# Optimization experiments

Measured on AMD Instinct MI355X. Metric: run time of the kernel, lower is better.

## Reference

```python
import jax, jax.numpy as jnp
from jax import lax
import numpy as np

B, S, D = 4, 4096, 1024
ESCAPE_RADIUS = 2.0  # Mandelbrot-style escape bound used for per-row clamping
EPS = 1e-12


def setup_inputs() -> dict:
    key = jax.random.key(0)
    ks = jax.random.split(key, 6)
    x = jax.random.normal(ks[0], (B, S, D), dtype=jnp.float32)
    gamma = jnp.ones((D,), dtype=jnp.float32)
    beta = jnp.zeros((D,), dtype=jnp.float32)
    scale = 1.0 / np.sqrt(D)
    W_in = jax.random.normal(ks[1], (D, D), dtype=jnp.float32) * scale
    b_in = jnp.zeros((D,), dtype=jnp.float32)
    W_out = jax.random.normal(ks[2], (D, D), dtype=jnp.float32) * scale
    b_out = jnp.zeros((D,), dtype=jnp.float32)
    return {"x": x, "gamma": gamma, "beta": beta, "W_in": W_in,
            "b_in": b_in, "W_out": W_out, "b_out": b_out}


def _layernorm(x, gamma, beta):
    mu = jnp.mean(x, axis=-1, keepdims=True)
    var = jnp.mean((x - mu) ** 2, axis=-1, keepdims=True)
    return (x - mu) * lax.rsqrt(var + 1e-5) * gamma + beta


def _complex_square(z):
    # last dim = [real | imag] halves (torch chunk(2, dim=-1))
    re, im = jnp.split(z, 2, axis=-1)
    return jnp.concatenate([re * re - im * im, 2.0 * re * im], axis=-1)


def reference(x, gamma, beta, W_in, b_in, W_out, b_out):
    h = _layernorm(x, gamma, beta)
    c = jnp.einsum('bsd,de->bse', h, W_in) + b_in  # per-token complex offset

    def step(z, c_t):
        z_raw = _complex_square(z) + c_t
        # per-row L2 norm clamp to escape radius (keeps the chaotic map bounded)
        n = jnp.sqrt(jnp.sum(z_raw * z_raw, axis=-1, keepdims=True) + EPS)
        z_new = z_raw * (ESCAPE_RADIUS / jnp.maximum(n, ESCAPE_RADIUS))
        return z_new, z_new

    c_t_major = jnp.swapaxes(c, 0, 1)  # [S, B, D]
    z0 = jnp.zeros((x.shape[0], x.shape[-1]), dtype=x.dtype)
    _, ys = lax.scan(step, z0, c_t_major)  # ys: [S, B, D]
    y = jnp.swapaxes(ys, 0, 1)  # [B, S, D]
    out = jnp.einsum('bsd,de->bse', y, W_out) + b_out
    return x + out  # residual
```

## Files before the change

### kernel.cpp

```cpp
#include <hip/hip_runtime.h>

typedef __bf16 bf16_t;
typedef float  f32x4  __attribute__((ext_vector_type(4)));
typedef long   longx2 __attribute__((ext_vector_type(2)));
typedef unsigned char u8;
typedef unsigned long long u64;

#define B_DIM 4
#define S_DIM 4096
#define D_DIM 1024
#define M_DIM (B_DIM * S_DIM)

#define CHUNK 32
#define WARM  16

__device__ __forceinline__ int pperm(int k) {
  return (k & ~63) | (((k >> 3) & 3) << 4) | (((k >> 5) & 1) << 3) | (k & 7);
}

__device__ __forceinline__ void g2l16(const void* g, void* l) {
  __builtin_amdgcn_global_load_lds(
      (const __attribute__((address_space(1))) void*)g,
      (__attribute__((address_space(3))) void*)l, 16, 0, 0);
}

__global__ __launch_bounds__(64) void ln_kernel(
    const float* __restrict__ x, const float* __restrict__ gamma,
    const float* __restrict__ beta, u8* __restrict__ h) {
  const int row  = blockIdx.x;
  const int lane = threadIdx.x;
  const float4* xr = (const float4*)(x + (size_t)row * D_DIM);
  float4 v[4];
  float s = 0.f, s2 = 0.f;
#pragma unroll
  for (int j = 0; j < 4; ++j) {
    v[j] = xr[j * 64 + lane];
    s += v[j].x + v[j].y + v[j].z + v[j].w;
    s2 = fmaf(v[j].x, v[j].x, s2);
    s2 = fmaf(v[j].y, v[j].y, s2);
    s2 = fmaf(v[j].z, v[j].z, s2);
    s2 = fmaf(v[j].w, v[j].w, s2);
  }
#pragma unroll
  for (int off = 32; off; off >>= 1) {
    s  += __shfl_xor(s, off);
    s2 += __shfl_xor(s2, off);
  }
  const float mu  = s * (1.f / (float)D_DIM);
  const float var = fmaf(-mu, mu, s2 * (1.f / (float)D_DIM));
  const float inv = rsqrtf(var + 1e-5f);
  int* hr = (int*)(h + (size_t)row * D_DIM);
#pragma unroll
  for (int j = 0; j < 4; ++j) {
    const float4 g4 = ((const float4*)gamma)[j * 64 + lane];
    const float4 b4 = ((const float4*)beta)[j * 64 + lane];
    const float o0 = fmaf((v[j].x - mu) * inv, g4.x, b4.x);
    const float o1 = fmaf((v[j].y - mu) * inv, g4.y, b4.y);
    const float o2 = fmaf((v[j].z - mu) * inv, g4.z, b4.z);
    const float o3 = fmaf((v[j].w - mu) * inv, g4.w, b4.w);
    int p = __builtin_amdgcn_cvt_pk_fp8_f32(o0, o1, 0, false);
    p = __builtin_amdgcn_cvt_pk_fp8_f32(o2, o3, p, true);
    hr[pperm(j * 256 + lane * 4) >> 2] = p;
  }
}

__global__ __launch_bounds__(256) void transpose_fp8_kernel(
    const float* __restrict__ W, u8* __restrict__ WT) {
  __shared__ float tile[32][33];
  const int tx = threadIdx.x & 31;
  const int ty = threadIdx.x >> 5;
  const int bn = blockIdx.x * 32;
  const int bk = blockIdx.y * 32;
#pragma unroll
  for (int i = 0; i < 32; i += 8)
    tile[ty + i][tx] = W[(size_t)(bk + ty + i) * D_DIM + bn + tx];
  __syncthreads();
#pragma unroll
  for (int i = 0; i < 32; i += 8) {
    const int p =
        __builtin_amdgcn_cvt_pk_fp8_f32(16.f * tile[tx][ty + i], 0.f, 0, false);
    WT[(size_t)(bn + ty + i) * D_DIM + pperm(bk + tx)] = (u8)(p & 0xff);
  }
}

#define NTK 16
#define BUFSZ 24576

#define VMCNT(n) asm volatile("s_waitcnt vmcnt(" #n ")" ::: "memory")
#define DSRX(d, a, off) \
  asm volatile("ds_read_b128 %0, %1 offset:" #off : "=v"(d) : "v"(a))

template <int MODE>
__global__ __launch_bounds__(512, 4) void gemm_fp8_kernel(
    const u8* __restrict__ A, const u8* __restrict__ BT,
    const float* __restrict__ bias, const float* __restrict__ xres,
    void* __restrict__ Cout) {
  __shared__ __attribute__((aligned(16))) char lds[3][BUFSZ];
  const int tid  = threadIdx.x;
  const int lane = tid & 63;
  const int wave = tid >> 6;
  const int wr = wave >> 2;
  const int wc = wave & 3;
  const int bid = blockIdx.x;
  const int swz = (bid & 7) * 64 + (bid >> 3);
  const int m0 = (swz >> 2) * 128;
  const int n0 = (swz & 3) * 256;

  const int dly = (int)((bid * 2654435761u) >> 29);
  for (int i = 0; i < dly; ++i) __builtin_amdgcn_s_sleep(1);

  const int us = (((tid & 3) ^ ((tid >> 3) & 3)) << 4);
  const u8* srcA = A  + (size_t)(m0 + (tid >> 2)) * D_DIM + us;
  const u8* srcB = BT + (size_t)(n0 + (tid >> 2)) * D_DIM + us;
  const int l16 = tid * 16;

  const uint32_t lbase = (uint32_t)(uintptr_t)&lds[0][0];
  const int sw = (((lane >> 4) ^ ((lane >> 1) & 3)) << 4);
  const uint32_t aoff = lbase + (uint32_t)((wr * 64 + (lane & 15)) * 64 + sw);
  const uint32_t boff = lbase + 8192u +
                        (uint32_t)((wc * 64 + (lane & 15)) * 64 + sw);

  f32x4 acc[4][4];
#pragma unroll
  for (int m = 0; m < 4; ++m)
#pragma unroll
    for (int n = 0; n < 4; ++n) acc[m][n] = (f32x4){0.f, 0.f, 0.f, 0.f};

#define STAGE(T, BI)                                           \
  {                                                            \
    char* dst = (char*)lds + (BI) * BUFSZ;                     \
    const size_t ko = (size_t)(T) * 64;                        \
    g2l16(srcA + ko, dst + l16);                               \
    g2l16(srcB + ko, dst + 8192 + l16);                        \
    g2l16(srcB + (size_t)128 * D_DIM + ko, dst + 16384 + l16); \
  }

#define STEP_BODY(CUR, DO_STAGE, T)                                 \
  {                                                                 \
    __builtin_amdgcn_s_barrier();                                   \
    const uint32_t bb = (uint32_t)(CUR) * BUFSZ;                    \
    longx2 af[4], bf[4];                                            \
    const uint32_t aA = aoff + bb;                                  \
    DSRX(af[0], aA, 0);                                             \
    DSRX(af[1], aA, 1024);                                          \
    DSRX(af[2], aA, 2048);                                          \
    DSRX(af[3], aA, 3072);                                          \
    const uint32_t bA = boff + bb;                                  \
    DSRX(bf[0], bA, 0);                                             \
    DSRX(bf[1], bA, 1024);                                          \
    DSRX(bf[2], bA, 2048);                                          \
    DSRX(bf[3], bA, 3072);                                          \
    if (DO_STAGE) { const int bi2 = (CUR) >= 1 ? (CUR) - 1 : (CUR) + 2; \
                    STAGE((T) + 2, bi2); }                          \
    asm volatile("s_waitcnt lgkmcnt(0)" ::: "memory");              \
    __builtin_amdgcn_sched_barrier(0);                              \
    _Pragma("unroll") for (int m = 0; m < 4; ++m)                   \
        _Pragma("unroll") for (int n = 0; n < 4; ++n)               \
            acc[m][n] = __builtin_amdgcn_mfma_f32_16x16x32_fp8_fp8( \
                af[m][0], bf[n][0], acc[m][n], 0, 0, 0);            \
    _Pragma("unroll") for (int m = 0; m < 4; ++m)                   \
        _Pragma("unroll") for (int n = 0; n < 4; ++n)               \
            acc[m][n] = __builtin_amdgcn_mfma_f32_16x16x32_fp8_fp8( \
                af[m][1], bf[n][1], acc[m][n], 0, 0, 0);            \
  }

  STAGE(0, 0);
  STAGE(1, 1);
  int cur = 0;
  for (int t = 0; t < NTK - 1; ++t) {
    VMCNT(3);
    STEP_BODY(cur, t + 2 < NTK, t);
    cur = cur == 2 ? 0 : cur + 1;
  }
  VMCNT(0);
  STEP_BODY(cur, false, NTK - 1);

#undef STEP_BODY
#undef STAGE

  const int rbase = m0 + wr * 64 + ((lane >> 4) << 2);
  const int cbase = n0 + wc * 64 + (lane & 15);
#pragma unroll
  for (int n = 0; n < 4; ++n) {
    const int col = cbase + n * 16;
    const float bn = bias[col];
#pragma unroll
    for (int m = 0; m < 4; ++m) {
      const int row = rbase + m * 16;
#pragma unroll
      for (int r = 0; r < 4; ++r) {
        const size_t idx = (size_t)(row + r) * D_DIM + col;
        if (MODE == 0) {
          const float cv = fmaf(acc[m][n][r], 0.0625f, bn);
          const int p = __builtin_amdgcn_cvt_pk_fp8_f32(cv, 0.f, 0, false);
          ((u8*)Cout)[idx] = (u8)(p & 0xff);
        } else {
          ((float*)Cout)[idx] =
              xres[idx] + fmaf(acc[m][n][r], 1.f / 256.f, bn);
        }
      }
    }
  }
}

__global__ __launch_bounds__(64) void scan_kernel(
    const u8* __restrict__ c, u8* __restrict__ y) {
  const int b     = blockIdx.y;
  const int chunk = blockIdx.x;
  const int t0    = chunk * CHUNK;
  const int start = (chunk == 0) ? 0 : t0 - WARM;
  const int tend  = t0 + CHUNK;
  const int lane  = threadIdx.x;

  float zre[8], zim[8];
#pragma unroll
  for (int j = 0; j < 8; ++j) { zre[j] = 0.f; zim[j] = 0.f; }

  const int dre = lane * 8;
  const int pre = (dre & ~63) | (((dre >> 3) & 3) << 4) | (((dre >> 5) & 1) << 3);
  const int pim = 512 + pre;

  const u8* crow = c + ((size_t)b * S_DIM + start) * D_DIM;
  u64 cr = *(const u64*)(crow + lane * 8);
  u64 ci = *(const u64*)(crow + 512 + lane * 8);

  for (int t = start; t < tend; ++t) {
    u64 crn = cr, cin = ci;
    if (t + 1 < tend) {
      const u8* nrow = c + ((size_t)b * S_DIM + (t + 1)) * D_DIM;
      crn = *(const u64*)(nrow + lane * 8);
      cin = *(const u64*)(nrow + 512 + lane * 8);
    }
    float cre[8], cim[8];
    {
      const unsigned rl = (unsigned)cr, rh = (unsigned)(cr >> 32);
      const unsigned il = (unsigned)ci, ih = (unsigned)(ci >> 32);
      cre[0] = __builtin_amdgcn_cvt_f32_fp8(rl, 0);
      cre[1] = __builtin_amdgcn_cvt_f32_fp8(rl, 1);
      cre[2] = __builtin_amdgcn_cvt_f32_fp8(rl, 2);
      cre[3] = __builtin_amdgcn_cvt_f32_fp8(rl, 3);
      cre[4] = __builtin_amdgcn_cvt_f32_fp8(rh, 0);
      cre[5] = __builtin_amdgcn_cvt_f32_fp8(rh, 1);
      cre[6] = __builtin_amdgcn_cvt_f32_fp8(rh, 2);
      cre[7] = __builtin_amdgcn_cvt_f32_fp8(rh, 3);
      cim[0] = __builtin_amdgcn_cvt_f32_fp8(il, 0);
      cim[1] = __builtin_amdgcn_cvt_f32_fp8(il, 1);
      cim[2] = __builtin_amdgcn_cvt_f32_fp8(il, 2);
      cim[3] = __builtin_amdgcn_cvt_f32_fp8(il, 3);
      cim[4] = __builtin_amdgcn_cvt_f32_fp8(ih, 0);
      cim[5] = __builtin_amdgcn_cvt_f32_fp8(ih, 1);
      cim[6] = __builtin_amdgcn_cvt_f32_fp8(ih, 2);
      cim[7] = __builtin_amdgcn_cvt_f32_fp8(ih, 3);
    }
    float nr[8], ni[8];
    float ss = 0.f;
#pragma unroll
    for (int j = 0; j < 8; ++j) {
      const float a  = zre[j], bb = zim[j];
      const float rr = fmaf(a, a, fmaf(-bb, bb, cre[j]));
      const float ii = fmaf(2.f * a, bb, cim[j]);
      nr[j] = rr; ni[j] = ii;
      ss = fmaf(rr, rr, ss);
      ss = fmaf(ii, ii, ss);
    }
#pragma unroll
    for (int off = 32; off; off >>= 1) ss += __shfl_xor(ss, off);
    const float nrm = sqrtf(ss + 1e-12f);
    const float sc  = 2.0f / fmaxf(nrm, 2.0f);
#pragma unroll
    for (int j = 0; j < 8; ++j) { zre[j] = nr[j] * sc; zim[j] = ni[j] * sc; }
    if (t >= t0) {
      u8* yrow = y + ((size_t)b * S_DIM + t) * D_DIM;
      int pr0 = __builtin_amdgcn_cvt_pk_fp8_f32(16.f * zre[0], 16.f * zre[1], 0, false);
      pr0 = __builtin_amdgcn_cvt_pk_fp8_f32(16.f * zre[2], 16.f * zre[3], pr0, true);
      int pr1 = __builtin_amdgcn_cvt_pk_fp8_f32(16.f * zre[4], 16.f * zre[5], 0, false);
      pr1 = __builtin_amdgcn_cvt_pk_fp8_f32(16.f * zre[6], 16.f * zre[7], pr1, true);
      int pi0 = __builtin_amdgcn_cvt_pk_fp8_f32(16.f * zim[0], 16.f * zim[1], 0, false);
      pi0 = __builtin_amdgcn_cvt_pk_fp8_f32(16.f * zim[2], 16.f * zim[3], pi0, true);
      int pi1 = __builtin_amdgcn_cvt_pk_fp8_f32(16.f * zim[4], 16.f * zim[5], 0, false);
      pi1 = __builtin_amdgcn_cvt_pk_fp8_f32(16.f * zim[6], 16.f * zim[7], pi1, true);
      *(u64*)(yrow + pre) = ((u64)(unsigned)pr1 << 32) | (unsigned)pr0;
      *(u64*)(yrow + pim) = ((u64)(unsigned)pi1 << 32) | (unsigned)pi0;
    }
    cr = crn; ci = cin;
  }
}

extern "C" void kernel_launch(void* const* d_in, const int* in_sizes, int n_in,
                              void* d_out, int out_size, void* d_ws, size_t ws_size,
                              hipStream_t stream) {
  const float* x     = (const float*)d_in[0];
  const float* gamma = (const float*)d_in[1];
  const float* beta  = (const float*)d_in[2];
  const float* W_in  = (const float*)d_in[3];
  const float* b_in  = (const float*)d_in[4];
  const float* W_out = (const float*)d_in[5];
  const float* b_out = (const float*)d_in[6];
  float* out = (float*)d_out;

  char* ws = (char*)d_ws;
  u8* hy8  = (u8*)(ws);
  u8* c8   = (u8*)(ws + (16ull << 20));
  u8* wti8 = (u8*)(ws + (64ull << 20));
  u8* wto8 = (u8*)(ws + (65ull << 20));

  transpose_fp8_kernel<<<dim3(32, 32), 256, 0, stream>>>(W_in, wti8);
  transpose_fp8_kernel<<<dim3(32, 32), 256, 0, stream>>>(W_out, wto8);
  ln_kernel<<<M_DIM, 64, 0, stream>>>(x, gamma, beta, hy8);
  gemm_fp8_kernel<0><<<512, 512, 0, stream>>>(hy8, wti8, b_in, nullptr, c8);
  scan_kernel<<<dim3(S_DIM / CHUNK, B_DIM), 64, 0, stream>>>(c8, hy8);
  gemm_fp8_kernel<1><<<512, 512, 0, stream>>>(hy8, wto8, b_out, x, out);
}
```

Measured before the change: 125.5 us.

## Load B operand directly into registers and shrink LDS to A-only staging

The FP8 GEMM no longer stages the B tile through LDS. Each wave now loads its B fragments straight from global memory into double-buffered registers, one K-step ahead, while A keeps a 3-slot LDS ring. This cuts LDS from three 24 KB buffers to three 8 KB buffers and removes the B LDS reads, aiming for better occupancy and less LDS traffic. The per-block randomized start-up sleep is also removed. The cost is that waves sharing the same columns now fetch B redundantly, using narrow strided global loads that depend on cache hits.

```diff
diff --git a/kernel.cpp b/kernel.cpp
--- a/kernel.cpp
+++ b/kernel.cpp
@@ -84,18 +84,19 @@
 }
 
 #define NTK 16
-#define BUFSZ 24576
 
 #define VMCNT(n) asm volatile("s_waitcnt vmcnt(" #n ")" ::: "memory")
 #define DSRX(d, a, off) \
   asm volatile("ds_read_b128 %0, %1 offset:" #off : "=v"(d) : "v"(a))
+#define GLB(d, a) \
+  asm volatile("global_load_dwordx4 %0, %1, off" : "=v"(d) : "v"(a) : "memory")
 
 template <int MODE>
 __global__ __launch_bounds__(512, 4) void gemm_fp8_kernel(
     const u8* __restrict__ A, const u8* __restrict__ BT,
     const float* __restrict__ bias, const float* __restrict__ xres,
     void* __restrict__ Cout) {
-  __shared__ __attribute__((aligned(16))) char lds[3][BUFSZ];
+  __shared__ __attribute__((aligned(16))) char lds[3][8192];
   const int tid  = threadIdx.x;
   const int lane = tid & 63;
   const int wave = tid >> 6;
@@ -106,19 +107,16 @@
   const int m0 = (swz >> 2) * 128;
   const int n0 = (swz & 3) * 256;
 
-  const int dly = (int)((bid * 2654435761u) >> 29);
-  for (int i = 0; i < dly; ++i) __builtin_amdgcn_s_sleep(1);
-
   const int us = (((tid & 3) ^ ((tid >> 3) & 3)) << 4);
-  const u8* srcA = A  + (size_t)(m0 + (tid >> 2)) * D_DIM + us;
-  const u8* srcB = BT + (size_t)(n0 + (tid >> 2)) * D_DIM + us;
+  const u8* srcA = A + (size_t)(m0 + (tid >> 2)) * D_DIM + us;
   const int l16 = tid * 16;
 
   const uint32_t lbase = (uint32_t)(uintptr_t)&lds[0][0];
   const int sw = (((lane >> 4) ^ ((lane >> 1) & 3)) << 4);
   const uint32_t aoff = lbase + (uint32_t)((wr * 64 + (lane & 15)) * 64 + sw);
-  const uint32_t boff = lbase + 8192u +
-                        (uint32_t)((wc * 64 + (lane & 15)) * 64 + sw);
+
+  const u8* bp = BT + (size_t)(n0 + wc * 64 + (lane & 15)) * D_DIM +
+                 ((lane >> 4) << 4);
 
   f32x4 acc[4][4];
 #pragma unroll
@@ -126,57 +124,58 @@
 #pragma unroll
     for (int n = 0; n < 4; ++n) acc[m][n] = (f32x4){0.f, 0.f, 0.f, 0.f};
 
-#define STAGE(T, BI)                                           \
-  {                                                            \
-    char* dst = (char*)lds + (BI) * BUFSZ;                     \
-    const size_t ko = (size_t)(T) * 64;                        \
-    g2l16(srcA + ko, dst + l16);                               \
-    g2l16(srcB + ko, dst + 8192 + l16);                        \
-    g2l16(srcB + (size_t)128 * D_DIM + ko, dst + 16384 + l16); \
-  }
-
-#define STEP_BODY(CUR, DO_STAGE, T)                                 \
-  {                                                                 \
-    __builtin_amdgcn_s_barrier();                                   \
-    const uint32_t bb = (uint32_t)(CUR) * BUFSZ;                    \
-    longx2 af[4], bf[4];                                            \
-    const uint32_t aA = aoff + bb;                                  \
-    DSRX(af[0], aA, 0);                                             \
-    DSRX(af[1], aA, 1024);                                          \
-    DSRX(af[2], aA, 2048);                                          \
-    DSRX(af[3], aA, 3072);                                          \
-    const uint32_t bA = boff + bb;                                  \
-    DSRX(bf[0], bA, 0);                                             \
-    DSRX(bf[1], bA, 1024);                                          \
-    DSRX(bf[2], bA, 2048);                                          \
-    DSRX(bf[3], bA, 3072);                                          \
-    if (DO_STAGE) { const int bi2 = (CUR) >= 1 ? (CUR) - 1 : (CUR) + 2; \
-                    STAGE((T) + 2, bi2); }                          \
-    asm volatile("s_waitcnt lgkmcnt(0)" ::: "memory");              \
-    __builtin_amdgcn_sched_barrier(0);                              \
-    _Pragma("unroll") for (int m = 0; m < 4; ++m)                   \
-        _Pragma("unroll") for (int n = 0; n < 4; ++n)               \
-            acc[m][n] = __builtin_amdgcn_mfma_f32_16x16x32_fp8_fp8( \
-                af[m][0], bf[n][0], acc[m][n], 0, 0, 0);            \
-    _Pragma("unroll") for (int m = 0; m < 4; ++m)                   \
-        _Pragma("unroll") for (int n = 0; n < 4; ++n)               \
-            acc[m][n] = __builtin_amdgcn_mfma_f32_16x16x32_fp8_fp8( \
-                af[m][1], bf[n][1], acc[m][n], 0, 0, 0);            \
-  }
-
-  STAGE(0, 0);
-  STAGE(1, 1);
-  int cur = 0;
-  for (int t = 0; t < NTK - 1; ++t) {
-    VMCNT(3);
-    STEP_BODY(cur, t + 2 < NTK, t);
-    cur = cur == 2 ? 0 : cur + 1;
-  }
-  VMCNT(0);
-  STEP_BODY(cur, false, NTK - 1);
-
-#undef STEP_BODY
-#undef STAGE
+#define STAGEA(T, SLOT) \
+  g2l16(srcA + (size_t)(T) * 64, (char*)lds + (SLOT) * 8192 + l16)
+
+#define LOADB(BF, T)                                        \
+  {                                                         \
+    const u64 a_ = (u64)(uintptr_t)(bp + (size_t)(T) * 64); \
+    GLB(BF[0], a_);                                         \
+    GLB(BF[1], a_ + 16384u);                                \
+    GLB(BF[2], a_ + 32768u);                                \
+    GLB(BF[3], a_ + 49152u);                                \
+  }
+
+#define ITER(T, BCUR, BNXT)                                            \
+  {                                                                    \
+    if ((T) < NTK - 1) { VMCNT(1); } else { VMCNT(0); }                \
+    __builtin_amdgcn_s_barrier();                                      \
+    asm volatile("" ::: "memory");                                     \
+    if ((T) + 1 < NTK) LOADB(BNXT, (T) + 1);                           \
+    if ((T) + 2 < NTK) STAGEA((T) + 2, ((T) + 2) % 3);                 \
+    __builtin_amdgcn_sched_barrier(0);                                 \
+    longx2 af[4];                                                      \
+    const uint32_t aA = aoff + (uint32_t)(((T) % 3) * 8192);           \
+    DSRX(af[0], aA, 0);                                                \
+    DSRX(af[1], aA, 1024);                                             \
+    DSRX(af[2], aA, 2048);                                             \
+    DSRX(af[3], aA, 3072);                                             \
+    asm volatile("s_waitcnt lgkmcnt(0)" ::: "memory");                 \
+    __builtin_amdgcn_sched_barrier(0);                                 \
+    _Pragma("unroll") for (int m = 0; m < 4; ++m)                      \
+        _Pragma("unroll") for (int n = 0; n < 4; ++n)                  \
+            acc[m][n] = __builtin_amdgcn_mfma_f32_16x16x32_fp8_fp8(    \
+                af[m][0], BCUR[n][0], acc[m][n], 0, 0, 0);             \
+    _Pragma("unroll") for (int m = 0; m < 4; ++m)                      \
+        _Pragma("unroll") for (int n = 0; n < 4; ++n)                  \
+            acc[m][n] = __builtin_amdgcn_mfma_f32_16x16x32_fp8_fp8(    \
+                af[m][1], BCUR[n][1], acc[m][n], 0, 0, 0);             \
+  }
+
+  longx2 bf_e[4], bf_o[4];
+  STAGEA(0, 0);
+  LOADB(bf_e, 0);
+  STAGEA(1, 1);
+
+#pragma unroll
+  for (int t2 = 0; t2 < NTK; t2 += 2) {
+    ITER(t2, bf_e, bf_o);
+    ITER(t2 + 1, bf_o, bf_e);
+  }
+
+#undef ITER
+#undef LOADB
+#undef STAGEA
 
   const int rbase = m0 + wr * 64 + ((lane >> 4) << 2);
   const int cbase = n0 + wc * 64 + (lane & 15);
```

New measurement: 162.0 us. 29.1% more time.
